# Kernel tuning notes

Hardware: AMD Instinct MI355X
Metric: run time of the kernel (lower is better)

Reference implementation:

```python
import jax, jax.numpy as jnp
import numpy as np

TAU_M = 4.0
TAU_S = 1.0
THRESH = 1.0
DECAY_M = float(np.exp(-1.0 / TAU_M))
EPS = 1e-5


@jax.custom_vjp
def spike_fn(v):
    return (v > THRESH).astype(v.dtype)


def _spike_fwd(v):
    return (v > THRESH).astype(v.dtype), v


def _spike_bwd(v, g):
    # rectangular surrogate gradient around the threshold
    return (g * (jnp.abs(v - THRESH) < 0.5).astype(g.dtype),)


spike_fn.defvjp(_spike_fwd, _spike_bwd)


def _axon(xt, a1, a2):
    # xt: [T, B, D]; second-order IIR: psp[t] = a1*psp[t-1] + a2*psp[t-2] + x[t]
    z = jnp.zeros(xt.shape[1:], xt.dtype)
    def step(c, xi):
        p1, p2 = c
        psp = a1 * p1 + a2 * p2 + xi
        return (psp, p1), psp
    _, out = jax.lax.scan(step, (z, z), xt)
    return out


def _lif(xt, W, b):
    # xt: [T, B, I] -> spikes [T, B, O]; LIF with hard reset
    z = jnp.einsum('tbi,oi->tbo', xt, W) + b
    z0 = jnp.zeros(z.shape[1:], z.dtype)
    def step(c, zt):
        v, s = c
        v = DECAY_M * v * (1.0 - s) + zt
        s = spike_fn(v)
        return (v, s), s
    _, out = jax.lax.scan(step, (z0, z0), z)
    return out


def _forward(inputs, W_mlp, b_mlp, gamma, beta, a1_1, a2_1, W1, b1,
             a1_2, a2_2, W2, b2, a1_3, a2_3, W3, b3, mask1, mask2):
    # per-timestep shared Linear: [B, 784, T]
    x = jnp.einsum('bit,oi->bot', inputs, W_mlp) + b_mlp[None, :, None]
    # BatchNorm1d (training-mode batch stats over batch and time per channel)
    mean = jnp.mean(x, axis=(0, 2), keepdims=True)
    var = jnp.var(x, axis=(0, 2), keepdims=True)
    x = gamma[None, :, None] * (x - mean) * jax.lax.rsqrt(var + EPS) + beta[None, :, None]
    x = jax.nn.sigmoid(x)
    xt = jnp.transpose(x, (2, 0, 1))  # [T, B, 784]
    h = _axon(xt, a1_1, a2_1)
    s1 = _lif(h, W1, b1) * jnp.transpose(mask1, (2, 0, 1))
    h = _axon(s1, a1_2, a2_2)
    s2 = _lif(h, W2, b2) * jnp.transpose(mask2, (2, 0, 1))
    h = _axon(s2, a1_3, a2_3)
    s3 = _lif(h, W3, b3)
    return jnp.transpose(s3, (1, 2, 0))  # [B, 10, T]


def setup_inputs() -> dict:
    key = jax.random.key(0)
    ks = jax.random.split(key, 8)
    B, D, T = 128, 784, 200
    H, O = 500, 10
    a1 = float(np.exp(-1.0 / TAU_M) + np.exp(-1.0 / TAU_S))
    a2 = float(-np.exp(-1.0 / TAU_M) * np.exp(-1.0 / TAU_S))
    def lin(k, o, i):
        return (jax.random.normal(k, (o, i), jnp.float32) / np.sqrt(i)).astype(jnp.float32)
    return {
        'inputs': jax.random.uniform(ks[0], (B, D, T), jnp.float32),
        'W_mlp': lin(ks[1], D, D),
        'b_mlp': jnp.zeros((D,), jnp.float32),
        'gamma': jnp.ones((D,), jnp.float32),
        'beta': jnp.zeros((D,), jnp.float32),
        'a1_1': jnp.full((D,), a1, jnp.float32),
        'a2_1': jnp.full((D,), a2, jnp.float32),
        'W1': lin(ks[2], H, D),
        'b1': jnp.zeros((H,), jnp.float32),
        'a1_2': jnp.full((H,), a1, jnp.float32),
        'a2_2': jnp.full((H,), a2, jnp.float32),
        'W2': lin(ks[3], H, H),
        'b2': jnp.zeros((H,), jnp.float32),
        'a1_3': jnp.full((H,), a1, jnp.float32),
        'a2_3': jnp.full((H,), a2, jnp.float32),
        'W3': lin(ks[4], O, H),
        'b3': jnp.zeros((O,), jnp.float32),
        'mask1': jax.random.bernoulli(ks[5], 0.7, (B, H, T)).astype(jnp.float32) / 0.7,
        'mask2': jax.random.bernoulli(ks[6], 0.7, (B, H, T)).astype(jnp.float32) / 0.7,
    }


def reference(inputs, W_mlp, b_mlp, gamma, beta, a1_1, a2_1, W1, b1,
              a1_2, a2_2, W2, b2, a1_3, a2_3, W3, b3, mask1, mask2):
    return _forward(inputs, W_mlp, b_mlp, gamma, beta, a1_1, a2_1, W1, b1,
                    a1_2, a2_2, W2, b2, a1_3, a2_3, W3, b3, mask1, mask2)
```

## Files before the change

kernel.cpp:

```cpp
#include <hip/hip_runtime.h>
#include <math.h>

typedef double f64x4 __attribute__((ext_vector_type(4)));

#define B_ 128
#define T_ 200
#define D_ 784
#define H_ 500
#define O_ 10
#define N_ROWS 25600
#define BD 100352
#define BH 64000
#define DECAY_M 0.77880078307140487f

#define OFF_BUFC   80281600ULL
#define OFF_BUFE   131481600ULL
#define OFF_STATS  132505600ULL
#define OFF_FLAGS  132518144ULL
#define WS_REQUIRED 132518272ULL

__global__ __launch_bounds__(256) void gemm_mfma(
    const float* __restrict__ A, const float* __restrict__ W,
    const float* __restrict__ bias, float* __restrict__ C,
    int N, int K, int M) {
  __shared__ float As[16][72];
  __shared__ float Bs[16][72];
  const int tid = threadIdx.x;
  const int lane = tid & 63;
  const int wave = tid >> 6;
  const int wr = (wave >> 1) * 32;
  const int wc = (wave & 1) * 32;
  const int l15 = lane & 15, lk = lane >> 4;
  const int n0 = blockIdx.y * 64;
  const int m0 = blockIdx.x * 64;

  f64x4 acc[2][2];
#pragma unroll
  for (int i = 0; i < 2; ++i)
#pragma unroll
    for (int j = 0; j < 2; ++j) acc[i][j] = f64x4{0.0, 0.0, 0.0, 0.0};

  const int srow = tid >> 2;
  const int sk4 = (tid & 3) << 2;
  const int Kt = (K + 15) >> 4;
  for (int kt = 0; kt < Kt; ++kt) {
    const int k0 = kt << 4;
    {
      int gc = k0 + sk4;
      float4 v = make_float4(0.f, 0.f, 0.f, 0.f);
      if (gc + 3 < K) v = *(const float4*)(A + (size_t)(n0 + srow) * K + gc);
      As[sk4 + 0][srow] = v.x; As[sk4 + 1][srow] = v.y;
      As[sk4 + 2][srow] = v.z; As[sk4 + 3][srow] = v.w;
    }
    {
      int gm = m0 + srow, gc = k0 + sk4;
      float4 v = make_float4(0.f, 0.f, 0.f, 0.f);
      if (gm < M && gc + 3 < K) v = *(const float4*)(W + (size_t)gm * K + gc);
      Bs[sk4 + 0][srow] = v.x; Bs[sk4 + 1][srow] = v.y;
      Bs[sk4 + 2][srow] = v.z; Bs[sk4 + 3][srow] = v.w;
    }
    __syncthreads();
    double af[2][4], bf[2][4];
#pragma unroll
    for (int i = 0; i < 2; ++i)
#pragma unroll
      for (int ks = 0; ks < 4; ++ks) {
        af[i][ks] = (double)As[ks * 4 + lk][wr + i * 16 + l15];
        bf[i][ks] = (double)Bs[ks * 4 + lk][wc + i * 16 + l15];
      }
#pragma unroll
    for (int ks = 0; ks < 4; ++ks)
#pragma unroll
      for (int i = 0; i < 2; ++i)
#pragma unroll
        for (int j = 0; j < 2; ++j)
          acc[i][j] = __builtin_amdgcn_mfma_f64_16x16x4f64(
              af[i][ks], bf[j][ks], acc[i][j], 0, 0, 0);
    __syncthreads();
  }
#pragma unroll
  for (int i = 0; i < 2; ++i)
#pragma unroll
    for (int j = 0; j < 2; ++j)
#pragma unroll
      for (int q = 0; q < 4; ++q) {
        int n = n0 + wr + i * 16 + q * 4 + lk;
        int m = m0 + wc + j * 16 + l15;
        if (m < M) C[(size_t)n * M + m] = (float)(acc[i][j][q] + (double)bias[m]);
      }
}

__global__ __launch_bounds__(256) void gemm1_mfma(
    const float* __restrict__ X, const float* __restrict__ W,
    const float* __restrict__ bias, float* __restrict__ C) {
  __shared__ float As[16][72];
  __shared__ float Bs[16][72];
  const int tid = threadIdx.x;
  const int lane = tid & 63;
  const int wave = tid >> 6;
  const int wr = (wave >> 1) * 32;
  const int wc = (wave & 1) * 32;
  const int l15 = lane & 15, lk = lane >> 4;
  const int n0 = blockIdx.y * 64;
  const int m0 = blockIdx.x * 64;

  f64x4 acc[2][2];
#pragma unroll
  for (int i = 0; i < 2; ++i)
#pragma unroll
    for (int j = 0; j < 2; ++j) acc[i][j] = f64x4{0.0, 0.0, 0.0, 0.0};

  const int arow = tid & 63;
  const int kq = tid >> 6;
  const int gr = n0 + arow;
  const int bb = gr / T_;
  const int tt = gr - bb * T_;
  const float* Abase = X + (size_t)bb * (D_ * T_) + tt;
  const int srow = tid >> 2;
  const int sk4 = (tid & 3) << 2;

  for (int kt = 0; kt < D_ / 16; ++kt) {
    const int k0 = kt << 4;
#pragma unroll
    for (int u = 0; u < 4; ++u) {
      int k = kq * 4 + u;
      As[k][arow] = Abase[(size_t)(k0 + k) * T_];
    }
    {
      int gm = m0 + srow, gc = k0 + sk4;
      float4 v = make_float4(0.f, 0.f, 0.f, 0.f);
      if (gm < D_) v = *(const float4*)(W + (size_t)gm * D_ + gc);
      Bs[sk4 + 0][srow] = v.x; Bs[sk4 + 1][srow] = v.y;
      Bs[sk4 + 2][srow] = v.z; Bs[sk4 + 3][srow] = v.w;
    }
    __syncthreads();
    double af[2][4], bf[2][4];
#pragma unroll
    for (int i = 0; i < 2; ++i)
#pragma unroll
      for (int ks = 0; ks < 4; ++ks) {
        af[i][ks] = (double)As[ks * 4 + lk][wr + i * 16 + l15];
        bf[i][ks] = (double)Bs[ks * 4 + lk][wc + i * 16 + l15];
      }
#pragma unroll
    for (int ks = 0; ks < 4; ++ks)
#pragma unroll
      for (int i = 0; i < 2; ++i)
#pragma unroll
        for (int j = 0; j < 2; ++j)
          acc[i][j] = __builtin_amdgcn_mfma_f64_16x16x4f64(
              af[i][ks], bf[j][ks], acc[i][j], 0, 0, 0);
    __syncthreads();
  }
#pragma unroll
  for (int i = 0; i < 2; ++i)
#pragma unroll
    for (int j = 0; j < 2; ++j)
#pragma unroll
      for (int q = 0; q < 4; ++q) {
        int n = n0 + wr + i * 16 + q * 4 + lk;
        int rb = n / T_;
        int rt = n - rb * T_;
        int m = m0 + wc + j * 16 + l15;
        if (m < D_)
          C[((size_t)rt * B_ + rb) * D_ + m] = (float)(acc[i][j][q] + (double)bias[m]);
      }
}

__global__ __launch_bounds__(256) void bn_stats(const float* __restrict__ Y,
                                                double* __restrict__ stats) {
  int col = blockIdx.x * 256 + threadIdx.x;
  int r0 = blockIdx.y * 256;
  if (col >= D_) return;
  double s = 0.0, s2 = 0.0;
  for (int rr = 0; rr < 256; ++rr) {
    float v = Y[(size_t)(r0 + rr) * D_ + col];
    s += v;
    s2 += (double)v * v;
  }
  atomicAdd(&stats[col], s);
  atomicAdd(&stats[D_ + col], s2);
}

__global__ __launch_bounds__(256) void bn_axon(
    float* __restrict__ Y, const double* __restrict__ stats,
    const float* __restrict__ gamma, const float* __restrict__ beta,
    const float* __restrict__ a1, const float* __restrict__ a2) {
  int j = blockIdx.x * 256 + threadIdx.x;
  int d = j % D_;
  double mean = stats[d] * (1.0 / N_ROWS);
  double var = stats[D_ + d] * (1.0 / N_ROWS) - mean * mean;
  float rstd = (float)(1.0 / sqrt(var + 1e-5));
  float mf = (float)mean;
  float g = gamma[d], be = beta[d];
  float c1 = a1[d], c2 = a2[d];
  float p1 = 0.f, p2 = 0.f;
  for (int t = 0; t < T_; ++t) {
    float x = Y[(size_t)t * BD + j];
    x = g * (x - mf) * rstd + be;
    x = 1.f / (1.f + expf(-x));
    float psp = c1 * p1 + c2 * p2 + x;
    Y[(size_t)t * BD + j] = psp;
    p2 = p1;
    p1 = psp;
  }
}

__global__ __launch_bounds__(256) void lif_axon(
    float* __restrict__ Z, const float* __restrict__ mask,
    const float* __restrict__ a1, const float* __restrict__ a2) {
  int j = blockIdx.x * 256 + threadIdx.x;
  int o = j % H_;
  float c1 = a1[o], c2 = a2[o];
  const float* mrow = mask + (size_t)j * T_;
  float v = 0.f, s = 0.f, p1 = 0.f, p2 = 0.f;
  for (int t = 0; t < T_; ++t) {
    float z = Z[(size_t)t * BH + j];
    v = DECAY_M * v * (1.f - s) + z;
    s = (v > 1.f) ? 1.f : 0.f;
    float sm = s * mrow[t];
    float psp = c1 * p1 + c2 * p2 + sm;
    Z[(size_t)t * BH + j] = psp;
    p2 = p1;
    p1 = psp;
  }
}

__global__ __launch_bounds__(256) void lif_out(const float* __restrict__ Z,
                                               float* __restrict__ out) {
  int j = blockIdx.x * 256 + threadIdx.x;
  if (j >= B_ * O_) return;
  float v = 0.f, s = 0.f;
  for (int t = 0; t < T_; ++t) {
    float z = Z[(size_t)t * (B_ * O_) + j];
    v = DECAY_M * v * (1.f - s) + z;
    s = (v > 1.f) ? 1.f : 0.f;
    out[(size_t)j * T_ + t] = s;
  }
}

__global__ void probe_ws(unsigned long long ws, float* flags) {
  if (ws < WS_REQUIRED) flags[0] = 9.0e6f;
}

__global__ __launch_bounds__(256) void probe_dot(
    const float* __restrict__ a, int sa, const float* __restrict__ w,
    const float* __restrict__ bias, const float* __restrict__ got,
    float sentinel, float* flags, int slot, int K) {
  __shared__ float red[256];
  float s = 0.f;
  for (int k = threadIdx.x; k < K; k += 256)
    s = fmaf(a[(size_t)k * sa], w[k], s);
  red[threadIdx.x] = s;
  __syncthreads();
  for (int h = 128; h > 0; h >>= 1) {
    if (threadIdx.x < h) red[threadIdx.x] += red[threadIdx.x + h];
    __syncthreads();
  }
  if (threadIdx.x == 0) {
    float want = red[0] + *bias;
    if (!(fabsf(*got - want) < 1e-2f)) flags[slot] = sentinel;
  }
}

__global__ void merge_flags(const float* __restrict__ flags, float* out) {
  int i = threadIdx.x;
  float f = flags[i];
  if (f != 0.0f) out[i] = f;
}

extern "C" void kernel_launch(void* const* d_in, const int* in_sizes, int n_in,
                              void* d_out, int out_size, void* d_ws, size_t ws_size,
                              hipStream_t stream) {
  const float* inputs = (const float*)d_in[0];
  const float* W_mlp  = (const float*)d_in[1];
  const float* b_mlp  = (const float*)d_in[2];
  const float* gamma  = (const float*)d_in[3];
  const float* beta   = (const float*)d_in[4];
  const float* a1_1   = (const float*)d_in[5];
  const float* a2_1   = (const float*)d_in[6];
  const float* W1     = (const float*)d_in[7];
  const float* b1     = (const float*)d_in[8];
  const float* a1_2   = (const float*)d_in[9];
  const float* a2_2   = (const float*)d_in[10];
  const float* W2     = (const float*)d_in[11];
  const float* b2     = (const float*)d_in[12];
  const float* a1_3   = (const float*)d_in[13];
  const float* a2_3   = (const float*)d_in[14];
  const float* W3     = (const float*)d_in[15];
  const float* b3     = (const float*)d_in[16];
  const float* mask1  = (const float*)d_in[17];
  const float* mask2  = (const float*)d_in[18];

  char* ws = (char*)d_ws;
  float* bufB  = (float*)ws;
  float* bufC  = (float*)(ws + OFF_BUFC);
  float* bufE  = (float*)(ws + OFF_BUFE);
  double* stats = (double*)(ws + OFF_STATS);
  float* flags = (float*)(ws + OFF_FLAGS);
  float* out = (float*)d_out;

  hipMemsetAsync(flags, 0, 64, stream);
  hipMemsetAsync(stats, 0, D_ * 2 * sizeof(double), stream);

  gemm1_mfma<<<dim3(13, 400), 256, 0, stream>>>(inputs, W_mlp, b_mlp, bufB);
  probe_dot<<<1, 256, 0, stream>>>(inputs + 11 * (D_ * T_) + 37, T_,
                                   W_mlp + 123 * D_, b_mlp + 123,
                                   bufB + (size_t)(37 * B_ + 11) * D_ + 123,
                                   8.0e6f, flags, 1, D_);

  bn_stats<<<dim3(4, 100), 256, 0, stream>>>(bufB, stats);
  bn_axon<<<BD / 256, 256, 0, stream>>>(bufB, stats, gamma, beta, a1_1, a2_1);

  gemm_mfma<<<dim3(8, 400), 256, 0, stream>>>(bufB, W1, b1, bufC, N_ROWS, D_, H_);
  probe_dot<<<1, 256, 0, stream>>>(bufB + (size_t)(91 * B_ + 77) * D_, 1,
                                   W1 + 333 * D_, b1 + 333,
                                   bufC + (size_t)(91 * B_ + 77) * H_ + 333,
                                   5.0e6f, flags, 3, D_);
  lif_axon<<<BH / 256, 256, 0, stream>>>(bufC, mask1, a1_2, a2_2);

  gemm_mfma<<<dim3(8, 400), 256, 0, stream>>>(bufC, W2, b2, bufB, N_ROWS, H_, H_);
  probe_dot<<<1, 256, 0, stream>>>(bufC + (size_t)(123 * B_ + 45) * H_, 1,
                                   W2 + 87 * H_, b2 + 87,
                                   bufB + (size_t)(123 * B_ + 45) * H_ + 87,
                                   3.0e6f, flags, 6, H_);
  lif_axon<<<BH / 256, 256, 0, stream>>>(bufB, mask2, a1_3, a2_3);

  gemm_mfma<<<dim3(1, 400), 256, 0, stream>>>(bufB, W3, b3, bufE, N_ROWS, H_, O_);
  probe_dot<<<1, 256, 0, stream>>>(bufB + (size_t)(11 * B_ + 99) * H_, 1,
                                   W3 + 7 * H_, b3 + 7,
                                   bufE + (size_t)(11 * B_ + 99) * O_ + 7,
                                   2.0e6f, flags, 7, H_);
  lif_out<<<5, 256, 0, stream>>>(bufE, out);

  probe_ws<<<1, 1, 0, stream>>>((unsigned long long)ws_size, flags);
  merge_flags<<<1, 16, 0, stream>>>(flags, out);
}
```

Measured before the change: 1.678 ms.

## Double-buffer LDS tiles in FP64 MFMA GEMMs with register prefetch and swizzle

Both GEMM kernels now keep two shared-memory tile buffers and prefetch the next K-tile's global loads into registers while the MFMA work runs on the current tile. The staged values are written to the other buffer afterward, which removes one barrier per iteration. Column indices are also XOR-style rotated by 16 on odd k-rows to reduce LDS bank conflicts on the transposed stores. The cost is twice the LDS footprint and more live registers, which could lower occupancy.

```diff
diff --git a/kernel.cpp b/kernel.cpp
--- a/kernel.cpp
+++ b/kernel.cpp
@@ -23,8 +23,8 @@
     const float* __restrict__ A, const float* __restrict__ W,
     const float* __restrict__ bias, float* __restrict__ C,
     int N, int K, int M) {
-  __shared__ float As[16][72];
-  __shared__ float Bs[16][72];
+  __shared__ float As[2][16][72];
+  __shared__ float Bs[2][16][72];
   const int tid = threadIdx.x;
   const int lane = tid & 63;
   const int wave = tid >> 6;
@@ -42,32 +42,50 @@
 
   const int srow = tid >> 2;
   const int sk4 = (tid & 3) << 2;
+  const int colW = (srow + ((tid & 1) << 4)) & 63;
+  int ca[2][2], cb[2][2];
+#pragma unroll
+  for (int i = 0; i < 2; ++i) {
+    int ra = wr + i * 16 + l15, rb = wc + i * 16 + l15;
+    ca[i][0] = ra; ca[i][1] = (ra + 16) & 63;
+    cb[i][0] = rb; cb[i][1] = (rb + 16) & 63;
+  }
+
+  const float* Arow = A + (size_t)(n0 + srow) * K;
+  const float* Wrow = W + (size_t)(m0 + srow) * K;
+  const bool wok = (m0 + srow) < M;
   const int Kt = (K + 15) >> 4;
+
+  {
+    float4 va = make_float4(0.f, 0.f, 0.f, 0.f), vb = va;
+    if (sk4 + 3 < K) va = *(const float4*)(Arow + sk4);
+    if (wok && sk4 + 3 < K) vb = *(const float4*)(Wrow + sk4);
+    As[0][sk4 + 0][colW] = va.x; As[0][sk4 + 1][colW] = va.y;
+    As[0][sk4 + 2][colW] = va.z; As[0][sk4 + 3][colW] = va.w;
+    Bs[0][sk4 + 0][colW] = vb.x; Bs[0][sk4 + 1][colW] = vb.y;
+    Bs[0][sk4 + 2][colW] = vb.z; Bs[0][sk4 + 3][colW] = vb.w;
+  }
+  __syncthreads();
+
   for (int kt = 0; kt < Kt; ++kt) {
-    const int k0 = kt << 4;
-    {
-      int gc = k0 + sk4;
-      float4 v = make_float4(0.f, 0.f, 0.f, 0.f);
-      if (gc + 3 < K) v = *(const float4*)(A + (size_t)(n0 + srow) * K + gc);
-      As[sk4 + 0][srow] = v.x; As[sk4 + 1][srow] = v.y;
-      As[sk4 + 2][srow] = v.z; As[sk4 + 3][srow] = v.w;
-    }
-    {
-      int gm = m0 + srow, gc = k0 + sk4;
-      float4 v = make_float4(0.f, 0.f, 0.f, 0.f);
-      if (gm < M && gc + 3 < K) v = *(const float4*)(W + (size_t)gm * K + gc);
-      Bs[sk4 + 0][srow] = v.x; Bs[sk4 + 1][srow] = v.y;
-      Bs[sk4 + 2][srow] = v.z; Bs[sk4 + 3][srow] = v.w;
-    }
-    __syncthreads();
+    const int cur = kt & 1;
+    const bool more = (kt + 1) < Kt;
+    float4 va = make_float4(0.f, 0.f, 0.f, 0.f), vb = va;
+    if (more) {
+      int gc = ((kt + 1) << 4) + sk4;
+      if (gc + 3 < K) va = *(const float4*)(Arow + gc);
+      if (wok && gc + 3 < K) vb = *(const float4*)(Wrow + gc);
+    }
     double af[2][4], bf[2][4];
 #pragma unroll
-    for (int i = 0; i < 2; ++i)
-#pragma unroll
-      for (int ks = 0; ks < 4; ++ks) {
-        af[i][ks] = (double)As[ks * 4 + lk][wr + i * 16 + l15];
-        bf[i][ks] = (double)Bs[ks * 4 + lk][wc + i * 16 + l15];
+    for (int ks = 0; ks < 4; ++ks) {
+      int kr = ks * 4 + lk, p = ks & 1;
+#pragma unroll
+      for (int i = 0; i < 2; ++i) {
+        af[i][ks] = (double)As[cur][kr][ca[i][p]];
+        bf[i][ks] = (double)Bs[cur][kr][cb[i][p]];
       }
+    }
 #pragma unroll
     for (int ks = 0; ks < 4; ++ks)
 #pragma unroll
@@ -76,6 +94,13 @@
         for (int j = 0; j < 2; ++j)
           acc[i][j] = __builtin_amdgcn_mfma_f64_16x16x4f64(
               af[i][ks], bf[j][ks], acc[i][j], 0, 0, 0);
+    if (more) {
+      int nb = cur ^ 1;
+      As[nb][sk4 + 0][colW] = va.x; As[nb][sk4 + 1][colW] = va.y;
+      As[nb][sk4 + 2][colW] = va.z; As[nb][sk4 + 3][colW] = va.w;
+      Bs[nb][sk4 + 0][colW] = vb.x; Bs[nb][sk4 + 1][colW] = vb.y;
+      Bs[nb][sk4 + 2][colW] = vb.z; Bs[nb][sk4 + 3][colW] = vb.w;
+    }
     __syncthreads();
   }
 #pragma unroll
@@ -93,8 +118,8 @@
 __global__ __launch_bounds__(256) void gemm1_mfma(
     const float* __restrict__ X, const float* __restrict__ W,
     const float* __restrict__ bias, float* __restrict__ C) {
-  __shared__ float As[16][72];
-  __shared__ float Bs[16][72];
+  __shared__ float As[2][16][72];
+  __shared__ float Bs[2][16][72];
   const int tid = threadIdx.x;
   const int lane = tid & 63;
   const int wave = tid >> 6;
@@ -112,36 +137,58 @@
 
   const int arow = tid & 63;
   const int kq = tid >> 6;
+  const int colWA = (arow + ((kq & 1) << 4)) & 63;
   const int gr = n0 + arow;
   const int bb = gr / T_;
   const int tt = gr - bb * T_;
   const float* Abase = X + (size_t)bb * (D_ * T_) + tt;
   const int srow = tid >> 2;
   const int sk4 = (tid & 3) << 2;
+  const int colWB = (srow + ((tid & 1) << 4)) & 63;
+  const float* Wrow = W + (size_t)(m0 + srow) * D_;
+  const bool wok = (m0 + srow) < D_;
+
+  int ca[2][2], cb[2][2];
+#pragma unroll
+  for (int i = 0; i < 2; ++i) {
+    int ra = wr + i * 16 + l15, rb = wc + i * 16 + l15;
+    ca[i][0] = ra; ca[i][1] = (ra + 16) & 63;
+    cb[i][0] = rb; cb[i][1] = (rb + 16) & 63;
+  }
+
+  {
+    float4 vb = make_float4(0.f, 0.f, 0.f, 0.f);
+    if (wok) vb = *(const float4*)(Wrow + sk4);
+#pragma unroll
+    for (int u = 0; u < 4; ++u)
+      As[0][kq * 4 + u][colWA] = Abase[(size_t)(kq * 4 + u) * T_];
+    Bs[0][sk4 + 0][colWB] = vb.x; Bs[0][sk4 + 1][colWB] = vb.y;
+    Bs[0][sk4 + 2][colWB] = vb.z; Bs[0][sk4 + 3][colWB] = vb.w;
+  }
+  __syncthreads();
 
   for (int kt = 0; kt < D_ / 16; ++kt) {
-    const int k0 = kt << 4;
-#pragma unroll
-    for (int u = 0; u < 4; ++u) {
-      int k = kq * 4 + u;
-      As[k][arow] = Abase[(size_t)(k0 + k) * T_];
-    }
-    {
-      int gm = m0 + srow, gc = k0 + sk4;
-      float4 v = make_float4(0.f, 0.f, 0.f, 0.f);
-      if (gm < D_) v = *(const float4*)(W + (size_t)gm * D_ + gc);
-      Bs[sk4 + 0][srow] = v.x; Bs[sk4 + 1][srow] = v.y;
-      Bs[sk4 + 2][srow] = v.z; Bs[sk4 + 3][srow] = v.w;
-    }
-    __syncthreads();
+    const int cur = kt & 1;
+    const bool more = (kt + 1) < D_ / 16;
+    float va[4];
+    float4 vb = make_float4(0.f, 0.f, 0.f, 0.f);
+    if (more) {
+      int k0 = (kt + 1) << 4;
+#pragma unroll
+      for (int u = 0; u < 4; ++u)
+        va[u] = Abase[(size_t)(k0 + kq * 4 + u) * T_];
+      if (wok) vb = *(const float4*)(Wrow + k0 + sk4);
+    }
     double af[2][4], bf[2][4];
 #pragma unroll
-    for (int i = 0; i < 2; ++i)
-#pragma unroll
-      for (int ks = 0; ks < 4; ++ks) {
-        af[i][ks] = (double)As[ks * 4 + lk][wr + i * 16 + l15];
-        bf[i][ks] = (double)Bs[ks * 4 + lk][wc + i * 16 + l15];
+    for (int ks = 0; ks < 4; ++ks) {
+      int kr = ks * 4 + lk, p = ks & 1;
+#pragma unroll
+      for (int i = 0; i < 2; ++i) {
+        af[i][ks] = (double)As[cur][kr][ca[i][p]];
+        bf[i][ks] = (double)Bs[cur][kr][cb[i][p]];
       }
+    }
 #pragma unroll
     for (int ks = 0; ks < 4; ++ks)
 #pragma unroll
@@ -150,6 +197,13 @@
         for (int j = 0; j < 2; ++j)
           acc[i][j] = __builtin_amdgcn_mfma_f64_16x16x4f64(
               af[i][ks], bf[j][ks], acc[i][j], 0, 0, 0);
+    if (more) {
+      int nb = cur ^ 1;
+#pragma unroll
+      for (int u = 0; u < 4; ++u) As[nb][kq * 4 + u][colWA] = va[u];
+      Bs[nb][sk4 + 0][colWB] = vb.x; Bs[nb][sk4 + 1][colWB] = vb.y;
+      Bs[nb][sk4 + 2][colWB] = vb.z; Bs[nb][sk4 + 3][colWB] = vb.w;
+    }
     __syncthreads();
   }
 #pragma unroll
```

Result: no change. 1.679 ms (+0.1%).
